# Performance work log

Hardware: AMD Instinct MI355X
Metric: run time of the kernel (lower is better)

Reference implementation:

```python
import jax, jax.numpy as jnp
import numpy as np

ALPHA = 0.2  # leaky_relu negative slope
NEG = -1e20


def gat_conv(x, edges, W, a, b):
    # x: [B,N,F], W: [F,O], a: [2O,1], b: [O]
    h = jnp.einsum('bnf,fo->bno', x, W)
    O = W.shape[1]
    # cat([h[src], h[tgt]]) @ a  ==  h[src]@a[:O] + h[tgt]@a[O:]
    s1 = h @ a[:O, 0]   # [B,N]
    s2 = h @ a[O:, 0]   # [B,N]
    src, tgt = edges[0], edges[1]
    e = jax.nn.leaky_relu(s1[:, src] + s2[:, tgt], ALPHA)  # [B,E]
    B, N, _ = h.shape
    # dense NxN scatter-assign, as in the original module
    att = jnp.full((B, N, N), NEG, dtype=h.dtype).at[:, src, tgt].set(e)
    att = jax.nn.softmax(att, axis=-1)
    return jnp.einsum('bnm,bmo->bno', att, h) + b


def setup_inputs() -> dict:
    key = jax.random.key(0)
    ks = jax.random.split(key, 8)
    B, N, E = 2, 2048, 32768
    Fin, nhid, nhead, Fout = 256, 8, 8, 64
    x = jax.random.normal(ks[0], (B, N, Fin), dtype=jnp.float32)
    edges = jax.random.randint(ks[1], (2, E), 0, N)
    # xavier-like init (gain 1.414)
    W_h = jax.random.normal(ks[2], (nhead, Fin, nhid), dtype=jnp.float32) * (1.414 / np.sqrt(Fin))
    a_h = jax.random.normal(ks[3], (nhead, 2 * nhid, 1), dtype=jnp.float32) * 0.3
    b_h = jnp.zeros((nhead, nhid), dtype=jnp.float32)
    W_o = jax.random.normal(ks[4], (nhid * nhead, Fout), dtype=jnp.float32) * (1.414 / np.sqrt(nhid * nhead))
    a_o = jax.random.normal(ks[5], (2 * Fout, 1), dtype=jnp.float32) * 0.1
    b_o = jnp.zeros((Fout,), dtype=jnp.float32)
    return {'x': x, 'edges': edges, 'W_h': W_h, 'a_h': a_h, 'b_h': b_h,
            'W_o': W_o, 'a_o': a_o, 'b_o': b_o}


def reference(x, edges, W_h, a_h, b_h, W_o, a_o, b_o):
    B, N, _ = x.shape
    # nhead parallel GATConv heads, concatenated along feature dim
    heads = jax.vmap(lambda W, a, b: gat_conv(x, edges, W, a, b))(W_h, a_h, b_h)  # [H,B,N,nhid]
    x1 = jax.nn.elu(jnp.moveaxis(heads, 0, 2).reshape(B, N, -1))  # [B,N,H*nhid]
    out = gat_conv(x1, edges, W_o, a_o, b_o)  # single out head (mean of 1)
    return jax.nn.log_softmax(out, axis=1)  # softmax over the node dim, per original
```

## Files before the change

### kernel.cpp

```cpp
#include <hip/hip_runtime.h>

#define BB   2
#define NN   2048
#define FIN  256
#define HH   8
#define NHID 8
#define C1   64
#define FOUT 64
#define MAXD 192
#define FASTD 64

__global__ __launch_bounds__(256)
void k_front(const float* __restrict__ x, const float* __restrict__ Wh,
             const float* __restrict__ ah, const int* __restrict__ edges, int E,
             float* __restrict__ h1, float* __restrict__ s1h, float* __restrict__ s2h,
             int* __restrict__ cnt, int* __restrict__ csr)
{
    __shared__ float xs[16][FIN];
    int tid = threadIdx.x;

    if (blockIdx.x >= 256) {
        int e = (blockIdx.x - 256) * 256 + tid;
        if (e < E) {
            int s = edges[e], t = edges[E + e];
            int pos = atomicAdd(&cnt[s], 1);
            if (pos < MAXD) csr[s * MAXD + pos] = t;
        }
        return;
    }

    int base = blockIdx.x * 16;
    const float4* xv = (const float4*)(x + (size_t)base * FIN);
    float4* xsv = (float4*)&xs[0][0];
#pragma unroll
    for (int i = 0; i < 4; ++i) xsv[tid + 256 * i] = xv[tid + 256 * i];
    __syncthreads();

    int wave = tid >> 6, lane = tid & 63;
    int head = lane >> 3, k = lane & 7;
    const float* Wp = Wh + head * FIN * NHID + k;
    int n0 = wave * 4;
    const float4* xr0 = (const float4*)xs[n0 + 0];
    const float4* xr1 = (const float4*)xs[n0 + 1];
    const float4* xr2 = (const float4*)xs[n0 + 2];
    const float4* xr3 = (const float4*)xs[n0 + 3];
    float a0 = 0.f, a1 = 0.f, a2 = 0.f, a3 = 0.f;
#pragma unroll 8
    for (int ff = 0; ff < FIN / 4; ++ff) {
        float4 v0 = xr0[ff], v1 = xr1[ff], v2 = xr2[ff], v3 = xr3[ff];
        float w0 = Wp[(4 * ff + 0) * NHID];
        float w1 = Wp[(4 * ff + 1) * NHID];
        float w2 = Wp[(4 * ff + 2) * NHID];
        float w3 = Wp[(4 * ff + 3) * NHID];
        a0 += w0 * v0.x; a0 += w1 * v0.y; a0 += w2 * v0.z; a0 += w3 * v0.w;
        a1 += w0 * v1.x; a1 += w1 * v1.y; a1 += w2 * v1.z; a1 += w3 * v1.w;
        a2 += w0 * v2.x; a2 += w1 * v2.y; a2 += w2 * v2.z; a2 += w3 * v2.w;
        a3 += w0 * v3.x; a3 += w1 * v3.y; a3 += w2 * v3.z; a3 += w3 * v3.w;
    }
    size_t hb = (size_t)(base + n0) * C1 + lane;
    h1[hb] = a0; h1[hb + C1] = a1; h1[hb + 2 * C1] = a2; h1[hb + 3 * C1] = a3;

    float c1 = ah[head * 16 + k], c2 = ah[head * 16 + 8 + k];
    float p0 = a0 * c1, p1 = a1 * c1, p2 = a2 * c1, p3 = a3 * c1;
    float q0 = a0 * c2, q1 = a1 * c2, q2 = a2 * c2, q3 = a3 * c2;
    for (int o = 1; o < 8; o <<= 1) {
        p0 += __shfl_xor(p0, o); p1 += __shfl_xor(p1, o);
        p2 += __shfl_xor(p2, o); p3 += __shfl_xor(p3, o);
        q0 += __shfl_xor(q0, o); q1 += __shfl_xor(q1, o);
        q2 += __shfl_xor(q2, o); q3 += __shfl_xor(q3, o);
    }
    if (k == 0) {
        float ps[4] = {p0, p1, p2, p3}, qs[4] = {q0, q1, q2, q3};
#pragma unroll
        for (int j = 0; j < 4; ++j) {
            int bn = base + n0 + j;
            int b = bn >> 11, n = bn & (NN - 1);
            s1h[(b * HH + head) * NN + n] = ps[j];
            s2h[(b * HH + head) * NN + n] = qs[j];
        }
    }
}

__global__ __launch_bounds__(256)
void k_att1g2(const float* __restrict__ h1, const float* __restrict__ s1h,
              const float* __restrict__ s2h, const float* __restrict__ bh,
              const int* __restrict__ cnt, int* __restrict__ csr,
              const float* __restrict__ Wo, const float* __restrict__ ao,
              float* __restrict__ h2, float* __restrict__ s1o, float* __restrict__ s2o)
{
    __shared__ int tg4[4][MAXD];
    __shared__ float es4[4][FASTD][HH];
    __shared__ float xs4[4][C1];
    int tid = threadIdx.x, w = tid >> 6, lane = tid & 63;
    int* tg = tg4[w];
    float* xs = xs4[w];
    int bn = blockIdx.x * 4 + w;
    int b = bn >> 11, n = bn & (NN - 1);
    int head = lane >> 3;

    int d = cnt[n]; if (d > MAXD) d = MAXD;
    for (int l = lane; l < d; l += 64) tg[l] = csr[n * MAXD + l];
    for (int l = lane; l < d; l += 64) {
        int t = tg[l], f = 0;
        for (int j = 0; j < l; ++j) f |= (tg[j] == t);
        if (f) tg[l] = -1;
    }
    for (int l = lane; l < d; l += 64) csr[n * MAXD + l] = tg[l];

    const float* hp = h1 + (size_t)b * NN * C1 + lane;
    float out;
    if (d == 0) {
        float acc = 0.f;
        for (int j = 0; j < NN; ++j) acc += hp[(size_t)j * C1];
        out = acc * (1.0f / NN);
    } else if (d <= FASTD) {
        const float* s2b = s2h + (size_t)b * HH * NN;
        for (int idx = lane; idx < d * HH; idx += 64) {
            int l = idx >> 3, hh = idx & 7;
            int t = tg[l];
            es4[w][l][hh] = s2b[hh * NN + (t < 0 ? 0 : t)];
        }
        float s1 = s1h[(b * HH + head) * NN + n];
        float m = -3.4e38f;
        for (int p = 0; p < d; ++p) {
            float ee = s1 + es4[w][p][head];
            ee = ee > 0.f ? ee : 0.2f * ee;
            m = fmaxf(m, tg[p] < 0 ? -3.4e38f : ee);
        }
        float den = 0.f, acc = 0.f;
        int p = 0;
        for (; p + 4 <= d; p += 4) {
            int t0 = tg[p], t1 = tg[p + 1], t2 = tg[p + 2], t3 = tg[p + 3];
            float v0 = hp[(size_t)(t0 < 0 ? 0 : t0) * C1];
            float v1 = hp[(size_t)(t1 < 0 ? 0 : t1) * C1];
            float v2 = hp[(size_t)(t2 < 0 ? 0 : t2) * C1];
            float v3 = hp[(size_t)(t3 < 0 ? 0 : t3) * C1];
            float e0 = s1 + es4[w][p + 0][head]; e0 = e0 > 0.f ? e0 : 0.2f * e0;
            float e1 = s1 + es4[w][p + 1][head]; e1 = e1 > 0.f ? e1 : 0.2f * e1;
            float e2 = s1 + es4[w][p + 2][head]; e2 = e2 > 0.f ? e2 : 0.2f * e2;
            float e3 = s1 + es4[w][p + 3][head]; e3 = e3 > 0.f ? e3 : 0.2f * e3;
            float w0 = t0 < 0 ? 0.f : expf(e0 - m);
            float w1 = t1 < 0 ? 0.f : expf(e1 - m);
            float w2 = t2 < 0 ? 0.f : expf(e2 - m);
            float w3 = t3 < 0 ? 0.f : expf(e3 - m);
            den += w0; acc += w0 * v0;
            den += w1; acc += w1 * v1;
            den += w2; acc += w2 * v2;
            den += w3; acc += w3 * v3;
        }
        for (; p < d; ++p) {
            int t = tg[p];
            float v = hp[(size_t)(t < 0 ? 0 : t) * C1];
            float ee = s1 + es4[w][p][head];
            ee = ee > 0.f ? ee : 0.2f * ee;
            float wt = t < 0 ? 0.f : expf(ee - m);
            den += wt; acc += wt * v;
        }
        out = acc / den;
    } else {
        float s1 = s1h[(b * HH + head) * NN + n];
        const float* s2p = s2h + (b * HH + head) * NN;
        float m = -3.4e38f;
        for (int p = 0; p < d; ++p) {
            int t = tg[p]; if (t < 0) continue;
            float ee = s1 + s2p[t];
            ee = ee > 0.f ? ee : 0.2f * ee;
            m = fmaxf(m, ee);
        }
        float den = 0.f, acc = 0.f;
        for (int p = 0; p < d; ++p) {
            int t = tg[p]; if (t < 0) continue;
            float ee = s1 + s2p[t];
            ee = ee > 0.f ? ee : 0.2f * ee;
            float wt = expf(ee - m);
            den += wt;
            acc += wt * hp[(size_t)t * C1];
        }
        out = acc / den;
    }
    out += bh[lane];
    xs[lane] = out > 0.f ? out : (expf(out) - 1.f);

    float acc2 = 0.f;
#pragma unroll 16
    for (int f = 0; f < C1; ++f) acc2 += xs[f] * Wo[f * FOUT + lane];
    h2[(size_t)bn * FOUT + lane] = acc2;
    float p = acc2 * ao[lane];
    float q = acc2 * ao[FOUT + lane];
    for (int o = 1; o < 64; o <<= 1) { p += __shfl_xor(p, o); q += __shfl_xor(q, o); }
    if (lane == 0) { s1o[bn] = p; s2o[bn] = q; }
}

__global__ __launch_bounds__(256)
void k_att2(const float* __restrict__ h2, const float* __restrict__ s1o,
            const float* __restrict__ s2o, const float* __restrict__ bo,
            const int* __restrict__ cnt, const int* __restrict__ csr,
            float* __restrict__ out2T)
{
    __shared__ int tg4[4][MAXD];
    __shared__ float es4[4][FASTD];
    int tid = threadIdx.x, w = tid >> 6, lane = tid & 63;
    int* tg = tg4[w];
    int bn = blockIdx.x * 4 + w;
    int b = bn >> 11, n = bn & (NN - 1);

    int d = cnt[n]; if (d > MAXD) d = MAXD;
    for (int l = lane; l < d; l += 64) tg[l] = csr[n * MAXD + l];

    const float* hp = h2 + (size_t)b * NN * FOUT + lane;
    const float* s2p = s2o + b * NN;
    float out;
    if (d == 0) {
        float acc = 0.f;
        for (int j = 0; j < NN; ++j) acc += hp[(size_t)j * FOUT];
        out = acc * (1.0f / NN);
    } else if (d <= FASTD) {
        for (int l = lane; l < d; l += 64) {
            int t = tg[l];
            es4[w][l] = s2p[t < 0 ? 0 : t];
        }
        float s1 = s1o[bn];
        float m = -3.4e38f;
        for (int p = 0; p < d; ++p) {
            float ee = s1 + es4[w][p];
            ee = ee > 0.f ? ee : 0.2f * ee;
            m = fmaxf(m, tg[p] < 0 ? -3.4e38f : ee);
        }
        float den = 0.f, acc = 0.f;
        int p = 0;
        for (; p + 4 <= d; p += 4) {
            int t0 = tg[p], t1 = tg[p + 1], t2 = tg[p + 2], t3 = tg[p + 3];
            float v0 = hp[(size_t)(t0 < 0 ? 0 : t0) * FOUT];
            float v1 = hp[(size_t)(t1 < 0 ? 0 : t1) * FOUT];
            float v2 = hp[(size_t)(t2 < 0 ? 0 : t2) * FOUT];
            float v3 = hp[(size_t)(t3 < 0 ? 0 : t3) * FOUT];
            float e0 = s1 + es4[w][p + 0]; e0 = e0 > 0.f ? e0 : 0.2f * e0;
            float e1 = s1 + es4[w][p + 1]; e1 = e1 > 0.f ? e1 : 0.2f * e1;
            float e2 = s1 + es4[w][p + 2]; e2 = e2 > 0.f ? e2 : 0.2f * e2;
            float e3 = s1 + es4[w][p + 3]; e3 = e3 > 0.f ? e3 : 0.2f * e3;
            float w0 = t0 < 0 ? 0.f : expf(e0 - m);
            float w1 = t1 < 0 ? 0.f : expf(e1 - m);
            float w2 = t2 < 0 ? 0.f : expf(e2 - m);
            float w3 = t3 < 0 ? 0.f : expf(e3 - m);
            den += w0; acc += w0 * v0;
            den += w1; acc += w1 * v1;
            den += w2; acc += w2 * v2;
            den += w3; acc += w3 * v3;
        }
        for (; p < d; ++p) {
            int t = tg[p];
            float v = hp[(size_t)(t < 0 ? 0 : t) * FOUT];
            float ee = s1 + es4[w][p];
            ee = ee > 0.f ? ee : 0.2f * ee;
            float wt = t < 0 ? 0.f : expf(ee - m);
            den += wt; acc += wt * v;
        }
        out = acc / den;
    } else {
        float s1 = s1o[bn];
        float m = -3.4e38f;
        for (int p = 0; p < d; ++p) {
            int t = tg[p]; if (t < 0) continue;
            float ee = s1 + s2p[t];
            ee = ee > 0.f ? ee : 0.2f * ee;
            m = fmaxf(m, ee);
        }
        float den = 0.f, acc = 0.f;
        for (int p = 0; p < d; ++p) {
            int t = tg[p]; if (t < 0) continue;
            float ee = s1 + s2p[t];
            ee = ee > 0.f ? ee : 0.2f * ee;
            float wt = expf(ee - m);
            den += wt;
            acc += wt * hp[(size_t)t * FOUT];
        }
        out = acc / den;
    }
    out2T[(size_t)(b * FOUT + lane) * NN + n] = out + bo[lane];
}

__global__ __launch_bounds__(256)
void k_lsef(const float* __restrict__ out2T, float* __restrict__ out)
{
    int row = blockIdx.x;
    int b = row >> 6, o = row & 63;
    int tid = threadIdx.x;
    const float* p = out2T + (size_t)row * NN;
    float v[8];
    float m = -3.4e38f;
#pragma unroll
    for (int j = 0; j < 8; ++j) {
        v[j] = p[tid + 256 * j];
        m = fmaxf(m, v[j]);
    }
    for (int off = 1; off < 64; off <<= 1) m = fmaxf(m, __shfl_xor(m, off));
    __shared__ float sm[4], ss[4];
    if ((tid & 63) == 0) sm[tid >> 6] = m;
    __syncthreads();
    float M = fmaxf(fmaxf(sm[0], sm[1]), fmaxf(sm[2], sm[3]));
    float sum = 0.f;
#pragma unroll
    for (int j = 0; j < 8; ++j) sum += expf(v[j] - M);
    for (int off = 1; off < 64; off <<= 1) sum += __shfl_xor(sum, off);
    if ((tid & 63) == 0) ss[tid >> 6] = sum;
    __syncthreads();
    float lse = M + logf(ss[0] + ss[1] + ss[2] + ss[3]);
    float* op = out + (size_t)b * NN * FOUT + o;
#pragma unroll
    for (int j = 0; j < 8; ++j) op[(size_t)(tid + 256 * j) * FOUT] = v[j] - lse;
}

extern "C" void kernel_launch(void* const* d_in, const int* in_sizes, int n_in,
                              void* d_out, int out_size, void* d_ws, size_t ws_size,
                              hipStream_t stream)
{
    (void)n_in; (void)out_size; (void)ws_size;
    const float* x     = (const float*)d_in[0];
    const int*   edges = (const int*)d_in[1];
    const float* Wh    = (const float*)d_in[2];
    const float* ah    = (const float*)d_in[3];
    const float* bh    = (const float*)d_in[4];
    const float* Wo    = (const float*)d_in[5];
    const float* ao    = (const float*)d_in[6];
    const float* bo    = (const float*)d_in[7];
    int E = in_sizes[1] / 2;

    char* w = (char*)d_ws;
    float* h1    = (float*)w; w += (size_t)BB * NN * C1 * 4;
    float* s1h   = (float*)w; w += (size_t)BB * HH * NN * 4;
    float* s2h   = (float*)w; w += (size_t)BB * HH * NN * 4;
    float* h2    = (float*)w; w += (size_t)BB * NN * FOUT * 4;
    float* s1o   = (float*)w; w += (size_t)BB * NN * 4;
    float* s2o   = (float*)w; w += (size_t)BB * NN * 4;
    float* out2T = (float*)w; w += (size_t)BB * FOUT * NN * 4;
    int*   cnt   = (int*)w;   w += (size_t)NN * 4;
    int*   csr   = (int*)w;   w += (size_t)NN * MAXD * 4;

    hipMemsetAsync(cnt, 0, (size_t)NN * 4, stream);

    int scatter_blocks = (E + 255) / 256;
    k_front <<<256 + scatter_blocks, 256, 0, stream>>>(x, Wh, ah, edges, E,
                                                       h1, s1h, s2h, cnt, csr);
    k_att1g2<<<BB * NN / 4, 256, 0, stream>>>(h1, s1h, s2h, bh, cnt, csr,
                                              Wo, ao, h2, s1o, s2o);
    k_att2  <<<BB * NN / 4, 256, 0, stream>>>(h2, s1o, s2o, bo, cnt, csr, out2T);
    k_lsef  <<<BB * FOUT, 256, 0, stream>>>(out2T, (float*)d_out);
}
```

Before: 113.7 us.

## Halve rows per front block and store attention scores node-major

The front GEMM now processes 8 nodes per block instead of 16, doubling the block count to 512 for more parallelism across the GPU. The s1h/s2h attention score buffers are transposed from [B,H,N] to [B,N,H], so the gather of all 8 heads for a neighbour in the attention kernel reads contiguous memory. The cost is less reuse of each W load per block and more blocks overall.

After: 111.4 us. 2.0% less time.

```diff
diff --git a/kernel.cpp b/kernel.cpp
--- a/kernel.cpp
+++ b/kernel.cpp
@@ -9,6 +9,7 @@
 #define FOUT 64
 #define MAXD 192
 #define FASTD 64
+#define GB1  512
 
 __global__ __launch_bounds__(256)
 void k_front(const float* __restrict__ x, const float* __restrict__ Wh,
@@ -16,11 +17,11 @@
              float* __restrict__ h1, float* __restrict__ s1h, float* __restrict__ s2h,
              int* __restrict__ cnt, int* __restrict__ csr)
 {
-    __shared__ float xs[16][FIN];
+    __shared__ float xs[8][FIN];
     int tid = threadIdx.x;
 
-    if (blockIdx.x >= 256) {
-        int e = (blockIdx.x - 256) * 256 + tid;
+    if (blockIdx.x >= GB1) {
+        int e = (blockIdx.x - GB1) * 256 + tid;
         if (e < E) {
             int s = edges[e], t = edges[E + e];
             int pos = atomicAdd(&cnt[s], 1);
@@ -29,54 +30,47 @@
         return;
     }
 
-    int base = blockIdx.x * 16;
+    int base = blockIdx.x * 8;
     const float4* xv = (const float4*)(x + (size_t)base * FIN);
     float4* xsv = (float4*)&xs[0][0];
-#pragma unroll
-    for (int i = 0; i < 4; ++i) xsv[tid + 256 * i] = xv[tid + 256 * i];
+    xsv[tid] = xv[tid];
+    xsv[tid + 256] = xv[tid + 256];
     __syncthreads();
 
     int wave = tid >> 6, lane = tid & 63;
     int head = lane >> 3, k = lane & 7;
     const float* Wp = Wh + head * FIN * NHID + k;
-    int n0 = wave * 4;
+    int n0 = wave * 2;
     const float4* xr0 = (const float4*)xs[n0 + 0];
     const float4* xr1 = (const float4*)xs[n0 + 1];
-    const float4* xr2 = (const float4*)xs[n0 + 2];
-    const float4* xr3 = (const float4*)xs[n0 + 3];
-    float a0 = 0.f, a1 = 0.f, a2 = 0.f, a3 = 0.f;
+    float a0 = 0.f, a1 = 0.f;
 #pragma unroll 8
     for (int ff = 0; ff < FIN / 4; ++ff) {
-        float4 v0 = xr0[ff], v1 = xr1[ff], v2 = xr2[ff], v3 = xr3[ff];
+        float4 v0 = xr0[ff], v1 = xr1[ff];
         float w0 = Wp[(4 * ff + 0) * NHID];
         float w1 = Wp[(4 * ff + 1) * NHID];
         float w2 = Wp[(4 * ff + 2) * NHID];
         float w3 = Wp[(4 * ff + 3) * NHID];
         a0 += w0 * v0.x; a0 += w1 * v0.y; a0 += w2 * v0.z; a0 += w3 * v0.w;
         a1 += w0 * v1.x; a1 += w1 * v1.y; a1 += w2 * v1.z; a1 += w3 * v1.w;
-        a2 += w0 * v2.x; a2 += w1 * v2.y; a2 += w2 * v2.z; a2 += w3 * v2.w;
-        a3 += w0 * v3.x; a3 += w1 * v3.y; a3 += w2 * v3.z; a3 += w3 * v3.w;
     }
     size_t hb = (size_t)(base + n0) * C1 + lane;
-    h1[hb] = a0; h1[hb + C1] = a1; h1[hb + 2 * C1] = a2; h1[hb + 3 * C1] = a3;
+    h1[hb] = a0; h1[hb + C1] = a1;
 
     float c1 = ah[head * 16 + k], c2 = ah[head * 16 + 8 + k];
-    float p0 = a0 * c1, p1 = a1 * c1, p2 = a2 * c1, p3 = a3 * c1;
-    float q0 = a0 * c2, q1 = a1 * c2, q2 = a2 * c2, q3 = a3 * c2;
+    float p0 = a0 * c1, p1 = a1 * c1;
+    float q0 = a0 * c2, q1 = a1 * c2;
     for (int o = 1; o < 8; o <<= 1) {
         p0 += __shfl_xor(p0, o); p1 += __shfl_xor(p1, o);
-        p2 += __shfl_xor(p2, o); p3 += __shfl_xor(p3, o);
         q0 += __shfl_xor(q0, o); q1 += __shfl_xor(q1, o);
-        q2 += __shfl_xor(q2, o); q3 += __shfl_xor(q3, o);
     }
     if (k == 0) {
-        float ps[4] = {p0, p1, p2, p3}, qs[4] = {q0, q1, q2, q3};
+        float ps[2] = {p0, p1}, qs[2] = {q0, q1};
 #pragma unroll
-        for (int j = 0; j < 4; ++j) {
+        for (int j = 0; j < 2; ++j) {
             int bn = base + n0 + j;
-            int b = bn >> 11, n = bn & (NN - 1);
-            s1h[(b * HH + head) * NN + n] = ps[j];
-            s2h[(b * HH + head) * NN + n] = qs[j];
+            s1h[(size_t)bn * HH + head] = ps[j];
+            s2h[(size_t)bn * HH + head] = qs[j];
         }
     }
 }
@@ -114,13 +108,13 @@
         for (int j = 0; j < NN; ++j) acc += hp[(size_t)j * C1];
         out = acc * (1.0f / NN);
     } else if (d <= FASTD) {
-        const float* s2b = s2h + (size_t)b * HH * NN;
+        const float* s2b = s2h + (size_t)b * NN * HH;
         for (int idx = lane; idx < d * HH; idx += 64) {
             int l = idx >> 3, hh = idx & 7;
             int t = tg[l];
-            es4[w][l][hh] = s2b[hh * NN + (t < 0 ? 0 : t)];
-        }
-        float s1 = s1h[(b * HH + head) * NN + n];
+            es4[w][l][hh] = s2b[(size_t)(t < 0 ? 0 : t) * HH + hh];
+        }
+        float s1 = s1h[(size_t)bn * HH + head];
         float m = -3.4e38f;
         for (int p = 0; p < d; ++p) {
             float ee = s1 + es4[w][p][head];
@@ -158,19 +152,19 @@
         }
         out = acc / den;
     } else {
-        float s1 = s1h[(b * HH + head) * NN + n];
-        const float* s2p = s2h + (b * HH + head) * NN;
+        float s1 = s1h[(size_t)bn * HH + head];
+        const float* s2b = s2h + (size_t)b * NN * HH;
         float m = -3.4e38f;
         for (int p = 0; p < d; ++p) {
             int t = tg[p]; if (t < 0) continue;
-            float ee = s1 + s2p[t];
+            float ee = s1 + s2b[(size_t)t * HH + head];
             ee = ee > 0.f ? ee : 0.2f * ee;
             m = fmaxf(m, ee);
         }
         float den = 0.f, acc = 0.f;
         for (int p = 0; p < d; ++p) {
             int t = tg[p]; if (t < 0) continue;
-            float ee = s1 + s2p[t];
+            float ee = s1 + s2b[(size_t)t * HH + head];
             ee = ee > 0.f ? ee : 0.2f * ee;
             float wt = expf(ee - m);
             den += wt;
@@ -327,8 +321,8 @@
 
     char* w = (char*)d_ws;
     float* h1    = (float*)w; w += (size_t)BB * NN * C1 * 4;
-    float* s1h   = (float*)w; w += (size_t)BB * HH * NN * 4;
-    float* s2h   = (float*)w; w += (size_t)BB * HH * NN * 4;
+    float* s1h   = (float*)w; w += (size_t)BB * NN * HH * 4;
+    float* s2h   = (float*)w; w += (size_t)BB * NN * HH * 4;
     float* h2    = (float*)w; w += (size_t)BB * NN * FOUT * 4;
     float* s1o   = (float*)w; w += (size_t)BB * NN * 4;
     float* s2o   = (float*)w; w += (size_t)BB * NN * 4;
@@ -339,7 +333,7 @@
     hipMemsetAsync(cnt, 0, (size_t)NN * 4, stream);
 
     int scatter_blocks = (E + 255) / 256;
-    k_front <<<256 + scatter_blocks, 256, 0, stream>>>(x, Wh, ah, edges, E,
+    k_front <<<GB1 + scatter_blocks, 256, 0, stream>>>(x, Wh, ah, edges, E,
                                                        h1, s1h, s2h, cnt, csr);
     k_att1g2<<<BB * NN / 4, 256, 0, stream>>>(h1, s1h, s2h, bh, cnt, csr,
                                               Wo, ao, h2, s1o, s2o);
```
